# Kernel tuning notes

Measured on AMD Instinct MI355X. Metric: run time of the kernel, lower is better.

Reference implementation:

```python
import jax, jax.numpy as jnp
import numpy as np

PSP_SIZES = (1, 3, 6, 8)
EPS = 1e-5  # BatchNorm eps (torch default)


def _adaptive_max_pool_flat(x, s):
    # Faithful torch AdaptiveMaxPool2d: window i is [floor(i*H/s), ceil((i+1)*H/s)).
    B, C, H, W = x.shape
    hs = [int(np.floor(i * H / s)) for i in range(s)]
    he = [int(np.ceil((i + 1) * H / s)) for i in range(s)]
    ws = [int(np.floor(j * W / s)) for j in range(s)]
    we = [int(np.ceil((j + 1) * W / s)) for j in range(s)]
    cells = []
    for i in range(s):  # small static loop (s <= 8)
        for j in range(s):
            cells.append(jnp.max(x[:, :, hs[i]:he[i], ws[j]:we[j]], axis=(2, 3)))
    return jnp.stack(cells, axis=-1)  # [B, C, s*s]


def _psp(x):
    return jnp.concatenate([_adaptive_max_pool_flat(x, s) for s in PSP_SIZES], axis=-1)  # [B, C, 110]


def _conv1x1(x, w):
    # x: [B, Cin, H, W], w: [Cout, Cin]
    return jnp.einsum('bchw,oc->bohw', x, w)


def _bn(y, gamma, beta, mean, var):
    inv = jax.lax.rsqrt(var + EPS)
    return (y - mean[None, :, None, None]) * (gamma * inv)[None, :, None, None] + beta[None, :, None, None]


def setup_inputs() -> dict:
    key = jax.random.key(0)
    ks = jax.random.split(key, 4)
    B, Cin, H, W = 8, 512, 64, 64
    Ck, Cv = 256, 512
    x = jax.random.normal(ks[0], (B, Cin, H, W), dtype=jnp.float32)
    qk_w = jax.random.normal(ks[1], (Ck, Cin), dtype=jnp.float32) * 0.02
    v_w = jax.random.normal(ks[2], (Cv, Cin), dtype=jnp.float32) * 0.02
    out_w = jax.random.normal(ks[3], (Cin, Cv), dtype=jnp.float32) * 0.02
    return {
        'x': x,
        'qk_w': qk_w, 'qk_gamma': jnp.ones(Ck), 'qk_beta': jnp.zeros(Ck),
        'qk_mean': jnp.zeros(Ck), 'qk_var': jnp.ones(Ck),
        'v_w': v_w, 'v_gamma': jnp.ones(Cv), 'v_beta': jnp.zeros(Cv),
        'v_mean': jnp.zeros(Cv), 'v_var': jnp.ones(Cv),
        'out_w': out_w, 'out_gamma': jnp.ones(Cin), 'out_beta': jnp.zeros(Cin),
        'out_mean': jnp.zeros(Cin), 'out_var': jnp.ones(Cin),
    }


def reference(x, qk_w, qk_gamma, qk_beta, qk_mean, qk_var,
              v_w, v_gamma, v_beta, v_mean, v_var,
              out_w, out_gamma, out_beta, out_mean, out_var):
    B, Cin, H, W = x.shape
    Ck = qk_w.shape[0]
    Cv = v_w.shape[0]
    # query_key branch: 1x1 conv + BN + ReLU
    qk = jax.nn.relu(_bn(_conv1x1(x, qk_w), qk_gamma, qk_beta, qk_mean, qk_var))  # [B,Ck,H,W]
    # value branch: 1x1 conv + BN + ReLU
    val = jax.nn.relu(_bn(_conv1x1(x, v_w), v_gamma, v_beta, v_mean, v_var))  # [B,Cv,H,W]
    key = _psp(qk)                          # [B, Ck, S=110]
    value = _psp(val).transpose(0, 2, 1)    # [B, S, Cv]
    query = qk.reshape(B, Ck, H * W).transpose(0, 2, 1)  # [B, N, Ck]
    scores = jnp.einsum('bnc,bcs->bns', query, key) * (Ck ** -0.5)  # [B, N, S]
    scores = jax.nn.softmax(scores, axis=-1)
    y = jnp.einsum('bns,bsc->bnc', scores, value)  # [B, N, Cv]
    y = y.transpose(0, 2, 1).reshape(B, Cv, H, W)
    y = _bn(_conv1x1(y, out_w), out_gamma, out_beta, out_mean, out_var)  # no activation
    return x + y
```

## Files before the change

### kernel.cpp

```cpp
#include <hip/hip_runtime.h>
#include <math.h>

#define B_    8
#define CIN   512
#define CK    256
#define CV    512
#define HW    4096
#define S_    110
#define SP    128
#define EPS   1e-5f

typedef __attribute__((ext_vector_type(8))) short bf16x8;
typedef __attribute__((ext_vector_type(4))) short bf16x4;
typedef __attribute__((ext_vector_type(4))) float f32x4;

__device__ __forceinline__ float b2f(short s) {
    unsigned int u = ((unsigned int)(unsigned short)s) << 16;
    union { unsigned int u; float f; } c; c.u = u; return c.f;
}
__device__ __forceinline__ short f2b(float f) {
    union { float f; unsigned int u; } c; c.f = f;
    unsigned int r = (c.u + 0x7FFFu + ((c.u >> 16) & 1u)) >> 16;
    return (short)r;
}

__device__ __forceinline__ void gload_lds16(const short* g, short* l) {
    __builtin_amdgcn_global_load_lds(
        (const __attribute__((address_space(1))) void*)g,
        (__attribute__((address_space(3))) void*)l,
        16, 0, 0);
}

template<int STRIDE>
__device__ __forceinline__ void stage_tile(
    const short* __restrict__ base, short* lds, int tid, int kt)
{
    const int wv = tid >> 6, lane = tid & 63;
    #pragma unroll
    for (int q = 0; q < 4; ++q) {
        const int u = q * 256 + wv * 64 + lane;
        const int row = u >> 3;
        const int kunit = (u & 7) ^ (row & 7);
        gload_lds16(base + (size_t)row * STRIDE + kt + kunit * 8,
                    lds + (q * 256 + wv * 64) * 8);
    }
}

__global__ __launch_bounds__(256) void transpose_x_kernel(
    const float* __restrict__ x, short* __restrict__ xt)
{
    __shared__ short t[64][65];
    const int b = blockIdx.z, c0 = blockIdx.y * 64, n0 = blockIdx.x * 64;
    const int tid = threadIdx.x;
    const float* src = x + ((size_t)b * CIN + c0) * HW + n0;
    const int j = tid & 63, i0 = tid >> 6;
    #pragma unroll
    for (int q = 0; q < 16; ++q) {
        int i = i0 * 16 + q;
        t[i][j] = f2b(src[(size_t)i * HW + j]);
    }
    __syncthreads();
    short* dst = xt + ((size_t)b * HW + n0) * CIN + c0;
    const int hh = tid & 31, jb = tid >> 5;
    #pragma unroll
    for (int q = 0; q < 8; ++q) {
        int jj = jb * 8 + q;
        short2 v; v.x = t[2 * hh][jj]; v.y = t[2 * hh + 1][jj];
        *(short2*)(dst + (size_t)jj * CIN + 2 * hh) = v;
    }
}

__global__ __launch_bounds__(256) void transpose_qk_kernel(
    const short* __restrict__ qkb, short* __restrict__ qkt)
{
    __shared__ short t[64][65];
    const int b = blockIdx.z, c0 = blockIdx.y * 64, n0 = blockIdx.x * 64;
    const int tid = threadIdx.x;
    const short* src = qkb + ((size_t)b * CK + c0) * HW + n0;
    const int j = tid & 63, i0 = tid >> 6;
    #pragma unroll
    for (int q = 0; q < 16; ++q) {
        int i = i0 * 16 + q;
        t[i][j] = src[(size_t)i * HW + j];
    }
    __syncthreads();
    short* dst = qkt + ((size_t)b * HW + n0) * CK + c0;
    const int hh = tid & 31, jb = tid >> 5;
    #pragma unroll
    for (int q = 0; q < 8; ++q) {
        int jj = jb * 8 + q;
        short2 v; v.x = t[2 * hh][jj]; v.y = t[2 * hh + 1][jj];
        *(short2*)(dst + (size_t)jj * CK + 2 * hh) = v;
    }
}

__global__ __launch_bounds__(256) void convert_w_kernel(
    const float* __restrict__ qk_w, const float* __restrict__ v_w,
    const float* __restrict__ out_w, short* __restrict__ wb)
{
    const int id4 = (blockIdx.x * 256 + threadIdx.x) * 4;
    #pragma unroll
    for (int r = 0; r < 4; ++r) {
        int id = id4 + r;
        float f = (id < 131072) ? qk_w[id]
                : (id < 393216) ? v_w[id - 131072]
                                : out_w[id - 393216];
        wb[id] = f2b(f);
    }
}

template<int MODE>
__global__ __launch_bounds__(256) void gemm_mfma_kernel(
    const short* __restrict__ W, const short* __restrict__ Bt,
    const float* __restrict__ g0, const float* __restrict__ be0,
    const float* __restrict__ mu0, const float* __restrict__ va0,
    const float* __restrict__ g1, const float* __restrict__ be1,
    const float* __restrict__ mu1, const float* __restrict__ va1,
    const float* __restrict__ xres,
    short* __restrict__ o0, short* __restrict__ o1,
    float* __restrict__ of)
{
    __shared__ short As[128 * 64];
    __shared__ short Bs[128 * 64];
    const int b   = blockIdx.z;
    const int mm0 = blockIdx.y * 128, nn0 = blockIdx.x * 128;
    const int tid = threadIdx.x;
    const int lane = tid & 63, wv = tid >> 6;
    const int wm = (wv >> 1) * 64, wn = (wv & 1) * 64;
    const int l15 = lane & 15, l4 = lane >> 4;

    const short* wbase = W + (size_t)mm0 * 512;
    const short* xbase = Bt + ((size_t)b * HW + nn0) * 512;

    f32x4 acc[4][4] = {};

    for (int kt = 0; kt < 512; kt += 64) {
        stage_tile<512>(wbase, As, tid, kt);
        stage_tile<512>(xbase, Bs, tid, kt);
        __syncthreads();
        #pragma unroll
        for (int kk = 0; kk < 2; ++kk) {
            bf16x8 af[4], bfr[4];
            #pragma unroll
            for (int m = 0; m < 4; ++m) {
                int row = wm + m * 16 + l15;
                int su = (kk * 4 + l4) ^ (row & 7);
                af[m] = *(const bf16x8*)&As[row * 64 + su * 8];
            }
            #pragma unroll
            for (int n = 0; n < 4; ++n) {
                int row = wn + n * 16 + l15;
                int su = (kk * 4 + l4) ^ (row & 7);
                bfr[n] = *(const bf16x8*)&Bs[row * 64 + su * 8];
            }
            #pragma unroll
            for (int m = 0; m < 4; ++m)
                #pragma unroll
                for (int n = 0; n < 4; ++n)
                    acc[m][n] = __builtin_amdgcn_mfma_f32_16x16x32_bf16(
                        af[m], bfr[n], acc[m][n], 0, 0, 0);
        }
        __syncthreads();
    }

    #pragma unroll
    for (int m = 0; m < 4; ++m) {
        #pragma unroll
        for (int i = 0; i < 4; ++i) {
            const int co = mm0 + wm + m * 16 + l4 * 4 + i;
            if (MODE == 0) {
                float sc, sh; short* dst;
                if (co < CK) {
                    sc = g0[co] * rsqrtf(va0[co] + EPS);
                    sh = be0[co] - mu0[co] * sc;
                    dst = o0 + ((size_t)b * CK + co) * HW;
                } else {
                    int cv = co - CK;
                    sc = g1[cv] * rsqrtf(va1[cv] + EPS);
                    sh = be1[cv] - mu1[cv] * sc;
                    dst = o1 + ((size_t)b * CV + cv) * HW;
                }
                #pragma unroll
                for (int n = 0; n < 4; ++n) {
                    float v = fmaxf(acc[m][n][i] * sc + sh, 0.f);
                    dst[nn0 + wn + n * 16 + l15] = f2b(v);
                }
            } else {
                float sc = g0[co] * rsqrtf(va0[co] + EPS);
                float sh = be0[co] - mu0[co] * sc;
                const float* xr = xres + ((size_t)b * CIN + co) * HW;
                float* orow = of + ((size_t)b * CIN + co) * HW;
                #pragma unroll
                for (int n = 0; n < 4; ++n) {
                    int nidx = nn0 + wn + n * 16 + l15;
                    orow[nidx] = acc[m][n][i] * sc + sh + xr[nidx];
                }
            }
        }
    }
}

__global__ __launch_bounds__(256) void psp_pool_kernel(
    const short* __restrict__ qkb, const short* __restrict__ valb,
    short* __restrict__ keyT, short* __restrict__ valueT)
{
    __shared__ float band[4][17][64];
    const int tid = threadIdx.x;
    const int lane = tid & 63, wv = tid >> 6;
    const int c = blockIdx.x * 4 + wv;
    const int b = blockIdx.y;

    const short* src = (c < CK) ? qkb + ((size_t)b * CK + c) * HW
                                : valb + ((size_t)b * CV + (c - CK)) * HW;

    const float NEG = -1e30f;
    float a0 = NEG;
    float b3[3] = {NEG, NEG, NEG};
    float c6[6] = {NEG, NEG, NEG, NEG, NEG, NEG};
    float d8[8] = {NEG, NEG, NEG, NEG, NEG, NEG, NEG, NEG};

    #pragma unroll
    for (int h = 0; h < 64; ++h) {
        float v = b2f(src[h * 64 + lane]);
        a0 = fmaxf(a0, v);
        if (h <= 21)            b3[0] = fmaxf(b3[0], v);
        if (h >= 21 && h <= 42) b3[1] = fmaxf(b3[1], v);
        if (h >= 42)            b3[2] = fmaxf(b3[2], v);
        if (h <= 10)            c6[0] = fmaxf(c6[0], v);
        if (h >= 10 && h <= 21) c6[1] = fmaxf(c6[1], v);
        if (h >= 21 && h <= 31) c6[2] = fmaxf(c6[2], v);
        if (h >= 32 && h <= 42) c6[3] = fmaxf(c6[3], v);
        if (h >= 42 && h <= 53) c6[4] = fmaxf(c6[4], v);
        if (h >= 53)            c6[5] = fmaxf(c6[5], v);
        d8[h >> 3] = fmaxf(d8[h >> 3], v);
    }

    #pragma unroll
    for (int r = 0; r < 3; ++r) band[wv][r][lane] = b3[r];
    #pragma unroll
    for (int r = 0; r < 6; ++r) band[wv][3 + r][lane] = c6[r];
    #pragma unroll
    for (int r = 0; r < 8; ++r) band[wv][9 + r][lane] = d8[r];

    #pragma unroll
    for (int off = 32; off; off >>= 1) a0 = fmaxf(a0, __shfl_xor(a0, off));

    __syncthreads();

    const int isK = (c < CK);
    const int cv = c - CK;

    if (lane == 0) {
        if (isK) keyT[((size_t)b * SP + 0) * CK + c] = f2b(a0);
        else     valueT[((size_t)b * CV + cv) * SP + 0] = f2b(a0);
    }
    {
        int i = lane >> 3, j = lane & 7;
        const float* row = band[wv][9 + i];
        float m = row[8 * j];
        #pragma unroll
        for (int k = 1; k < 8; ++k) m = fmaxf(m, row[8 * j + k]);
        int sc = 46 + lane;
        if (isK) keyT[((size_t)b * SP + sc) * CK + c] = f2b(m);
        else     valueT[((size_t)b * CV + cv) * SP + sc] = f2b(m);
    }
    if (lane < 36) {
        int i = lane / 6, j = lane - 6 * i;
        int w0 = (j * 64) / 6, w1 = ((j + 1) * 64 + 5) / 6;
        const float* row = band[wv][3 + i];
        float m = NEG;
        for (int k = w0; k < w1; ++k) m = fmaxf(m, row[k]);
        int sc = 10 + lane;
        if (isK) keyT[((size_t)b * SP + sc) * CK + c] = f2b(m);
        else     valueT[((size_t)b * CV + cv) * SP + sc] = f2b(m);
    }
    if (lane < 9) {
        int i = lane / 3, j = lane - 3 * i;
        int w0 = (j * 64) / 3, w1 = ((j + 1) * 64 + 2) / 3;
        const float* row = band[wv][i];
        float m = NEG;
        for (int k = w0; k < w1; ++k) m = fmaxf(m, row[k]);
        int sc = 1 + lane;
        if (isK) keyT[((size_t)b * SP + sc) * CK + c] = f2b(m);
        else     valueT[((size_t)b * CV + cv) * SP + sc] = f2b(m);
    }
}

__global__ __launch_bounds__(256) void attn_scores_mfma_kernel(
    const short* __restrict__ qkt, const short* __restrict__ keyT,
    short* __restrict__ P)
{
    __shared__ short As[128 * 64];
    __shared__ short Bs[128 * 64];
    __shared__ float red[2][2][128];
    const int b  = blockIdx.y;
    const int m0 = blockIdx.x * 128;
    const int tid = threadIdx.x;
    const int lane = tid & 63, wv = tid >> 6;
    const int wm = (wv >> 1) * 64, wn = (wv & 1) * 64;
    const int l15 = lane & 15, l4 = lane >> 4;

    const short* abase = qkt + ((size_t)b * HW + m0) * CK;
    const short* bbase = keyT + (size_t)b * SP * CK;

    f32x4 acc[4][4] = {};

    for (int kt = 0; kt < CK; kt += 64) {
        stage_tile<CK>(abase, As, tid, kt);
        stage_tile<CK>(bbase, Bs, tid, kt);
        __syncthreads();
        #pragma unroll
        for (int kk = 0; kk < 2; ++kk) {
            bf16x8 af[4], bfr[4];
            #pragma unroll
            for (int m = 0; m < 4; ++m) {
                int row = wm + m * 16 + l15;
                int su = (kk * 4 + l4) ^ (row & 7);
                af[m] = *(const bf16x8*)&As[row * 64 + su * 8];
            }
            #pragma unroll
            for (int n = 0; n < 4; ++n) {
                int row = wn + n * 16 + l15;
                int su = (kk * 4 + l4) ^ (row & 7);
                bfr[n] = *(const bf16x8*)&Bs[row * 64 + su * 8];
            }
            #pragma unroll
            for (int m = 0; m < 4; ++m)
                #pragma unroll
                for (int n = 0; n < 4; ++n)
                    acc[m][n] = __builtin_amdgcn_mfma_f32_16x16x32_bf16(
                        af[m], bfr[n], acc[m][n], 0, 0, 0);
        }
        __syncthreads();
    }

    float pv[4][4][4];
    float rmax[4][4], rsum[4][4];
    #pragma unroll
    for (int m = 0; m < 4; ++m)
        #pragma unroll
        for (int i = 0; i < 4; ++i) {
            float mx = -1e30f;
            #pragma unroll
            for (int n = 0; n < 4; ++n) {
                int s = wn + n * 16 + l15;
                float v = acc[m][n][i] * 0.0625f;
                if (s >= S_) v = -1e30f;
                pv[m][n][i] = v;
                mx = fmaxf(mx, v);
            }
            rmax[m][i] = mx;
        }
    #pragma unroll
    for (int off = 1; off < 16; off <<= 1)
        #pragma unroll
        for (int m = 0; m < 4; ++m)
            #pragma unroll
            for (int i = 0; i < 4; ++i)
                rmax[m][i] = fmaxf(rmax[m][i], __shfl_xor(rmax[m][i], off));
    if (l15 == 0) {
        #pragma unroll
        for (int m = 0; m < 4; ++m)
            #pragma unroll
            for (int i = 0; i < 4; ++i)
                red[0][wv & 1][wm + m * 16 + l4 * 4 + i] = rmax[m][i];
    }
    __syncthreads();
    #pragma unroll
    for (int m = 0; m < 4; ++m)
        #pragma unroll
        for (int i = 0; i < 4; ++i) {
            float gmax = fmaxf(rmax[m][i], red[0][(wv & 1) ^ 1][wm + m * 16 + l4 * 4 + i]);
            float sm = 0.f;
            #pragma unroll
            for (int n = 0; n < 4; ++n) {
                float e = __expf(pv[m][n][i] - gmax);
                pv[m][n][i] = e;
                sm += e;
            }
            rsum[m][i] = sm;
        }
    #pragma unroll
    for (int off = 1; off < 16; off <<= 1)
        #pragma unroll
        for (int m = 0; m < 4; ++m)
            #pragma unroll
            for (int i = 0; i < 4; ++i)
                rsum[m][i] += __shfl_xor(rsum[m][i], off);
    if (l15 == 0) {
        #pragma unroll
        for (int m = 0; m < 4; ++m)
            #pragma unroll
            for (int i = 0; i < 4; ++i)
                red[1][wv & 1][wm + m * 16 + l4 * 4 + i] = rsum[m][i];
    }
    __syncthreads();
    #pragma unroll
    for (int m = 0; m < 4; ++m)
        #pragma unroll
        for (int i = 0; i < 4; ++i) {
            int row = wm + m * 16 + l4 * 4 + i;
            float inv = 1.f / (rsum[m][i] + red[1][(wv & 1) ^ 1][row]);
            short* dst = P + ((size_t)b * HW + m0 + row) * SP + wn + l15;
            #pragma unroll
            for (int n = 0; n < 4; ++n)
                dst[n * 16] = f2b(pv[m][n][i] * inv);
        }
}

__global__ __launch_bounds__(256) void attn_pv_mfma_kernel(
    const short* __restrict__ P, const short* __restrict__ valueT,
    short* __restrict__ Yt)
{
    __shared__ short As[128 * 64];
    __shared__ short Bs[128 * 64];
    const int b   = blockIdx.z;
    const int m0  = blockIdx.y * 128;
    const int cv0 = blockIdx.x * 128;
    const int tid = threadIdx.x;
    const int lane = tid & 63, wv = tid >> 6;
    const int wm = (wv >> 1) * 64, wn = (wv & 1) * 64;
    const int l15 = lane & 15, l4 = lane >> 4;

    const short* abase = P + ((size_t)b * HW + m0) * SP;
    const short* bbase = valueT + ((size_t)b * CV + cv0) * SP;

    f32x4 acc[4][4] = {};

    for (int kt = 0; kt < SP; kt += 64) {
        stage_tile<SP>(abase, As, tid, kt);
        stage_tile<SP>(bbase, Bs, tid, kt);
        __syncthreads();
        #pragma unroll
        for (int kk = 0; kk < 2; ++kk) {
            bf16x8 af[4], bfr[4];
            #pragma unroll
            for (int m = 0; m < 4; ++m) {
                int row = wm + m * 16 + l15;
                int su = (kk * 4 + l4) ^ (row & 7);
                af[m] = *(const bf16x8*)&As[row * 64 + su * 8];
            }
            #pragma unroll
            for (int n = 0; n < 4; ++n) {
                int row = wn + n * 16 + l15;
                int su = (kk * 4 + l4) ^ (row & 7);
                bfr[n] = *(const bf16x8*)&Bs[row * 64 + su * 8];
            }
            #pragma unroll
            for (int m = 0; m < 4; ++m)
                #pragma unroll
                for (int n = 0; n < 4; ++n)
                    acc[m][n] = __builtin_amdgcn_mfma_f32_16x16x32_bf16(
                        af[m], bfr[n], acc[m][n], 0, 0, 0);
        }
        __syncthreads();
    }

    #pragma unroll
    for (int m = 0; m < 4; ++m)
        #pragma unroll
        for (int i = 0; i < 4; ++i) {
            int row = wm + m * 16 + l4 * 4 + i;
            short* dst = Yt + ((size_t)b * HW + m0 + row) * CV + cv0 + wn + l15;
            #pragma unroll
            for (int n = 0; n < 4; ++n)
                dst[n * 16] = f2b(acc[m][n][i]);
        }
}

extern "C" void kernel_launch(void* const* d_in, const int* in_sizes, int n_in,
                              void* d_out, int out_size, void* d_ws, size_t ws_size,
                              hipStream_t stream)
{
    const float* x        = (const float*)d_in[0];
    const float* qk_w     = (const float*)d_in[1];
    const float* qk_gamma = (const float*)d_in[2];
    const float* qk_beta  = (const float*)d_in[3];
    const float* qk_mean  = (const float*)d_in[4];
    const float* qk_var   = (const float*)d_in[5];
    const float* v_w      = (const float*)d_in[6];
    const float* v_gamma  = (const float*)d_in[7];
    const float* v_beta   = (const float*)d_in[8];
    const float* v_mean   = (const float*)d_in[9];
    const float* v_var    = (const float*)d_in[10];
    const float* out_w    = (const float*)d_in[11];
    const float* out_gamma= (const float*)d_in[12];
    const float* out_beta = (const float*)d_in[13];
    const float* out_mean = (const float*)d_in[14];
    const float* out_var  = (const float*)d_in[15];

    char* wsb = (char*)d_ws;
    short* xt     = (short*)(wsb);
    short* qkt    = xt;
    short* qkb    = (short*)(wsb + 33554432);
    short* valb   = (short*)(wsb + 50331648);
    short* Yt     = valb;
    short* keyT   = (short*)(wsb + 83886080);
    short* valueT = (short*)(wsb + 84410368);
    short* P      = (short*)(wsb + 85458944);
    short* wqkv   = (short*)(wsb + 93847552);
    short* wout   = wqkv + 393216;

    transpose_x_kernel<<<dim3(HW / 64, CIN / 64, B_), 256, 0, stream>>>(x, xt);
    convert_w_kernel<<<dim3(640), 256, 0, stream>>>(qk_w, v_w, out_w, wqkv);

    gemm_mfma_kernel<0><<<dim3(HW / 128, 6, B_), 256, 0, stream>>>(
        wqkv, xt, qk_gamma, qk_beta, qk_mean, qk_var,
        v_gamma, v_beta, v_mean, v_var,
        nullptr, qkb, valb, nullptr);

    transpose_qk_kernel<<<dim3(HW / 64, CK / 64, B_), 256, 0, stream>>>(qkb, qkt);

    psp_pool_kernel<<<dim3((CK + CV) / 4, B_), 256, 0, stream>>>(qkb, valb, keyT, valueT);

    attn_scores_mfma_kernel<<<dim3(HW / 128, B_), 256, 0, stream>>>(qkt, keyT, P);

    attn_pv_mfma_kernel<<<dim3(CV / 128, HW / 128, B_), 256, 0, stream>>>(P, valueT, Yt);

    gemm_mfma_kernel<1><<<dim3(HW / 128, 4, B_), 256, 0, stream>>>(
        wout, Yt, out_gamma, out_beta, out_mean, out_var,
        nullptr, nullptr, nullptr, nullptr,
        x, nullptr, nullptr, (float*)d_out);
}
```

Baseline: 272.7 us.

## Double-buffer LDS tiles in all MFMA GEMM kernels to overlap loads with compute

Replaces the single-buffered stage/sync/compute loop in the three MFMA GEMM kernels with a shared double-buffered gemm_loop. The next K tile is issued via global_load_lds into the alternate buffer while MFMAs consume the current one, which also removes one barrier per iteration. LDS use per block doubles to 64 KB, which can lower occupancy. Correctness depends on the barrier placement ordering the async LDS writes against reads of the other buffer.

Measured after the change: 269.8 us. No clear change (-1.0%).

```diff
diff --git a/kernel.cpp b/kernel.cpp
--- a/kernel.cpp
+++ b/kernel.cpp
@@ -43,6 +43,60 @@
         const int kunit = (u & 7) ^ (row & 7);
         gload_lds16(base + (size_t)row * STRIDE + kt + kunit * 8,
                     lds + (q * 256 + wv * 64) * 8);
+    }
+}
+
+__device__ __forceinline__ void mfma_step(
+    const short* As, const short* Bs, int wm, int wn, int l15, int l4,
+    f32x4 acc[4][4])
+{
+    #pragma unroll
+    for (int kk = 0; kk < 2; ++kk) {
+        bf16x8 af[4], bfr[4];
+        #pragma unroll
+        for (int m = 0; m < 4; ++m) {
+            int row = wm + m * 16 + l15;
+            int su = (kk * 4 + l4) ^ (row & 7);
+            af[m] = *(const bf16x8*)&As[row * 64 + su * 8];
+        }
+        #pragma unroll
+        for (int n = 0; n < 4; ++n) {
+            int row = wn + n * 16 + l15;
+            int su = (kk * 4 + l4) ^ (row & 7);
+            bfr[n] = *(const bf16x8*)&Bs[row * 64 + su * 8];
+        }
+        #pragma unroll
+        for (int m = 0; m < 4; ++m)
+            #pragma unroll
+            for (int n = 0; n < 4; ++n)
+                acc[m][n] = __builtin_amdgcn_mfma_f32_16x16x32_bf16(
+                    af[m], bfr[n], acc[m][n], 0, 0, 0);
+    }
+}
+
+template<int NK, int SA, int SB>
+__device__ __forceinline__ void gemm_loop(
+    const short* __restrict__ abase, const short* __restrict__ bbase,
+    short* As0, short* As1, short* Bs0, short* Bs1,
+    int tid, int wm, int wn, int l15, int l4, f32x4 acc[4][4])
+{
+    stage_tile<SA>(abase, As0, tid, 0);
+    stage_tile<SB>(bbase, Bs0, tid, 0);
+    __syncthreads();
+    #pragma unroll
+    for (int t = 0; t < NK; t += 2) {
+        if (t + 1 < NK) {
+            stage_tile<SA>(abase, As1, tid, (t + 1) * 64);
+            stage_tile<SB>(bbase, Bs1, tid, (t + 1) * 64);
+        }
+        mfma_step(As0, Bs0, wm, wn, l15, l4, acc);
+        __syncthreads();
+        if (t + 2 < NK) {
+            stage_tile<SA>(abase, As0, tid, (t + 2) * 64);
+            stage_tile<SB>(bbase, Bs0, tid, (t + 2) * 64);
+        }
+        mfma_step(As1, Bs1, wm, wn, l15, l4, acc);
+        __syncthreads();
     }
 }
 
@@ -120,8 +174,8 @@
     short* __restrict__ o0, short* __restrict__ o1,
     float* __restrict__ of)
 {
-    __shared__ short As[128 * 64];
-    __shared__ short Bs[128 * 64];
+    __shared__ short As[2][128 * 64];
+    __shared__ short Bs[2][128 * 64];
     const int b   = blockIdx.z;
     const int mm0 = blockIdx.y * 128, nn0 = blockIdx.x * 128;
     const int tid = threadIdx.x;
@@ -133,35 +187,8 @@
     const short* xbase = Bt + ((size_t)b * HW + nn0) * 512;
 
     f32x4 acc[4][4] = {};
-
-    for (int kt = 0; kt < 512; kt += 64) {
-        stage_tile<512>(wbase, As, tid, kt);
-        stage_tile<512>(xbase, Bs, tid, kt);
-        __syncthreads();
-        #pragma unroll
-        for (int kk = 0; kk < 2; ++kk) {
-            bf16x8 af[4], bfr[4];
-            #pragma unroll
-            for (int m = 0; m < 4; ++m) {
-                int row = wm + m * 16 + l15;
-                int su = (kk * 4 + l4) ^ (row & 7);
-                af[m] = *(const bf16x8*)&As[row * 64 + su * 8];
-            }
-            #pragma unroll
-            for (int n = 0; n < 4; ++n) {
-                int row = wn + n * 16 + l15;
-                int su = (kk * 4 + l4) ^ (row & 7);
-                bfr[n] = *(const bf16x8*)&Bs[row * 64 + su * 8];
-            }
-            #pragma unroll
-            for (int m = 0; m < 4; ++m)
-                #pragma unroll
-                for (int n = 0; n < 4; ++n)
-                    acc[m][n] = __builtin_amdgcn_mfma_f32_16x16x32_bf16(
-                        af[m], bfr[n], acc[m][n], 0, 0, 0);
-        }
-        __syncthreads();
-    }
+    gemm_loop<8, 512, 512>(wbase, xbase, As[0], As[1], Bs[0], Bs[1],
+                           tid, wm, wn, l15, l4, acc);
 
     #pragma unroll
     for (int m = 0; m < 4; ++m) {
@@ -290,8 +317,8 @@
     const short* __restrict__ qkt, const short* __restrict__ keyT,
     short* __restrict__ P)
 {
-    __shared__ short As[128 * 64];
-    __shared__ short Bs[128 * 64];
+    __shared__ short As[2][128 * 64];
+    __shared__ short Bs[2][128 * 64];
     __shared__ float red[2][2][128];
     const int b  = blockIdx.y;
     const int m0 = blockIdx.x * 128;
@@ -304,35 +331,8 @@
     const short* bbase = keyT + (size_t)b * SP * CK;
 
     f32x4 acc[4][4] = {};
-
-    for (int kt = 0; kt < CK; kt += 64) {
-        stage_tile<CK>(abase, As, tid, kt);
-        stage_tile<CK>(bbase, Bs, tid, kt);
-        __syncthreads();
-        #pragma unroll
-        for (int kk = 0; kk < 2; ++kk) {
-            bf16x8 af[4], bfr[4];
-            #pragma unroll
-            for (int m = 0; m < 4; ++m) {
-                int row = wm + m * 16 + l15;
-                int su = (kk * 4 + l4) ^ (row & 7);
-                af[m] = *(const bf16x8*)&As[row * 64 + su * 8];
-            }
-            #pragma unroll
-            for (int n = 0; n < 4; ++n) {
-                int row = wn + n * 16 + l15;
-                int su = (kk * 4 + l4) ^ (row & 7);
-                bfr[n] = *(const bf16x8*)&Bs[row * 64 + su * 8];
-            }
-            #pragma unroll
-            for (int m = 0; m < 4; ++m)
-                #pragma unroll
-                for (int n = 0; n < 4; ++n)
-                    acc[m][n] = __builtin_amdgcn_mfma_f32_16x16x32_bf16(
-                        af[m], bfr[n], acc[m][n], 0, 0, 0);
-        }
-        __syncthreads();
-    }
+    gemm_loop<4, CK, CK>(abase, bbase, As[0], As[1], Bs[0], Bs[1],
+                         tid, wm, wn, l15, l4, acc);
 
     float pv[4][4][4];
     float rmax[4][4], rsum[4][4];
@@ -412,8 +412,8 @@
     const short* __restrict__ P, const short* __restrict__ valueT,
     short* __restrict__ Yt)
 {
-    __shared__ short As[128 * 64];
-    __shared__ short Bs[128 * 64];
+    __shared__ short As[2][128 * 64];
+    __shared__ short Bs[2][128 * 64];
     const int b   = blockIdx.z;
     const int m0  = blockIdx.y * 128;
     const int cv0 = blockIdx.x * 128;
@@ -426,35 +426,8 @@
     const short* bbase = valueT + ((size_t)b * CV + cv0) * SP;
 
     f32x4 acc[4][4] = {};
-
-    for (int kt = 0; kt < SP; kt += 64) {
-        stage_tile<SP>(abase, As, tid, kt);
-        stage_tile<SP>(bbase, Bs, tid, kt);
-        __syncthreads();
-        #pragma unroll
-        for (int kk = 0; kk < 2; ++kk) {
-            bf16x8 af[4], bfr[4];
-            #pragma unroll
-            for (int m = 0; m < 4; ++m) {
-                int row = wm + m * 16 + l15;
-                int su = (kk * 4 + l4) ^ (row & 7);
-                af[m] = *(const bf16x8*)&As[row * 64 + su * 8];
-            }
-            #pragma unroll
-            for (int n = 0; n < 4; ++n) {
-                int row = wn + n * 16 + l15;
-                int su = (kk * 4 + l4) ^ (row & 7);
-                bfr[n] = *(const bf16x8*)&Bs[row * 64 + su * 8];
-            }
-            #pragma unroll
-            for (int m = 0; m < 4; ++m)
-                #pragma unroll
-                for (int n = 0; n < 4; ++n)
-                    acc[m][n] = __builtin_amdgcn_mfma_f32_16x16x32_bf16(
-                        af[m], bfr[n], acc[m][n], 0, 0, 0);
-        }
-        __syncthreads();
-    }
+    gemm_loop<2, SP, SP>(abase, bbase, As[0], As[1], Bs[0], Bs[1],
+                         tid, wm, wn, l15, l4, acc);
 
     #pragma unroll
     for (int m = 0; m < 4; ++m)
```
